# Optimization experiments

Measured on AMD Instinct MI355X. Metric: run time of the kernel, lower is better.

The kernel has to match this reference:

```python
import jax, jax.numpy as jnp
import numpy as np

COMMITMENT_COST = 0.25
FMAX = jnp.finfo(jnp.float32).max


def _vq(x, codebook, commitment_cost):
    """Eval-mode VectorQuantizerEMA forward. x: [T, B, D], codebook: [K, D]."""
    K, D = codebook.shape
    flat = x.reshape(-1, D)  # [N, D]
    dist = (jnp.sum(flat * flat, axis=1, keepdims=True)
            + jnp.sum(codebook * codebook, axis=1)
            - 2.0 * flat @ codebook.T)
    idx = jnp.argmin(dist, axis=1)                      # [N]
    quantized = codebook[idx].reshape(x.shape)          # gather instead of one-hot matmul
    e_latent_loss = jnp.mean((jax.lax.stop_gradient(quantized) - x) ** 2)
    loss = commitment_cost * e_latent_loss
    q_st = x + jax.lax.stop_gradient(quantized - x)     # straight-through
    counts = jnp.zeros((K,), dtype=x.dtype).at[idx].add(1.0)
    avg_probs = counts / flat.shape[0]
    perplexity = jnp.exp(-jnp.sum(avg_probs * jnp.log(avg_probs + 1e-10)))
    return loss, q_st, perplexity, idx, dist


def setup_inputs() -> dict:
    key = jax.random.key(0)
    k1, k2, k3 = jax.random.split(key, 3)
    Tp1, B, D = 257, 64, 768
    Kc, Kf = 512, 4096
    return {
        "features": jax.random.normal(k1, (Tp1, B, D), dtype=jnp.float32),
        "class_codebook": jax.random.normal(k2, (Kc, D), dtype=jnp.float32),
        "feat_codebook": jax.random.normal(k3, (Kf, D), dtype=jnp.float32),
    }


def reference(features, class_codebook, feat_codebook):
    Kc = class_codebook.shape[0]
    Kf = feat_codebook.shape[0]
    B = features.shape[1]

    # class quantization on features[0][None] -> [1, B, D]
    c_loss, q_class, c_perp, c_idx, c_dist = _vq(features[0][None], class_codebook, COMMITMENT_COST)
    # feature quantization on features[1:] -> [T, B, D]
    f_loss, q_feat, f_perp, f_idx, f_dist = _vq(features[1:], feat_codebook, COMMITMENT_COST)

    T = q_feat.shape[0]
    class_indices = c_idx.reshape(1, B)
    feature_indices = (f_idx + Kc).reshape(T, B)

    class_distances = c_dist.reshape(1, B, Kc)
    feature_distances = f_dist.reshape(T, B, Kf)
    # pad each with float32 max so argmin stays within own codebook range
    class_distances = jnp.concatenate(
        [class_distances, jnp.full((1, B, Kf), FMAX, dtype=jnp.float32)], axis=-1)
    feature_distances = jnp.concatenate(
        [jnp.full((T, B, Kc), FMAX, dtype=jnp.float32), feature_distances], axis=-1)
    distances = jnp.concatenate([class_distances, feature_distances], axis=0)  # [T+1, B, Kc+Kf]
    distances = jnp.transpose(distances, (1, 0, 2))                            # [B, T+1, Kc+Kf]

    encoding_indices = jnp.concatenate([class_indices, feature_indices], axis=0).reshape(-1, 1)
    quantized_features = jnp.concatenate([q_class, q_feat], axis=0)            # [T+1, B, D]

    loss = f_loss + c_loss
    perplexity = f_perp + c_perp
    return loss, quantized_features, perplexity, encoding_indices, distances
```

## Files before the change

kernel.cpp:

```cpp
#include <hip/hip_runtime.h>
#include <math.h>

#define DD 768
#define BB 64
#define TT 256
#define TP1 257
#define KCLS 512
#define KFEAT 4096
#define KSUM 4608
#define NROW_F 16384
#define NROW_ALL 16448

#define OFF_Q 1
#define OFF_PERP 12632065
#define OFF_IDX 12632066
#define OFF_DIST 12648514
#define PADV 3.0e38f

#define WS_COUNTS 0
#define WS_LOSS 4608
#define WS_XSQ 4736
#define WS_ESQ 21184
#define WSB_AMIN 103168ULL
#define WSB_AH   234752ULL
#define WSB_BH   25400576ULL

typedef __attribute__((ext_vector_type(8))) short bf16x8;
typedef __attribute__((ext_vector_type(4))) float f32x4;
typedef unsigned long long u64;

__device__ __forceinline__ unsigned short f2bf(float f) {
  unsigned u = __float_as_uint(f);
  unsigned r = (u + 0x7fff + ((u >> 16) & 1)) >> 16;
  return (unsigned short)r;
}
__device__ __forceinline__ void gload16(void* l, const void* g) {
  __builtin_amdgcn_global_load_lds((const __attribute__((address_space(1))) void*)g,
                                   (__attribute__((address_space(3))) void*)l, 16, 0, 0);
}

#define NA4 3145728
#define NB4 786432
__global__ __launch_bounds__(256) void convert_k(const float* __restrict__ A,
                                                 const float* __restrict__ B,
                                                 ushort* __restrict__ Ah,
                                                 ushort* __restrict__ Bh) {
  int i = blockIdx.x * 256 + threadIdx.x;
  const float4* src; ushort* dh; int j;
  if (i < NA4) { src = (const float4*)A; j = i; dh = Ah; }
  else { src = (const float4*)B; j = i - NA4; dh = Bh; }
  float4 v = src[j];
  ushort4 h;
  h.x = f2bf(v.x); h.y = f2bf(v.y); h.z = f2bf(v.z); h.w = f2bf(v.w);
  ((ushort4*)dh)[j] = h;
}

__global__ __launch_bounds__(256) void norms_k(const float* __restrict__ feats,
                                               const float* __restrict__ ccb,
                                               const float* __restrict__ fcb,
                                               float* __restrict__ ws) {
  int wv = (blockIdx.x << 2) + (threadIdx.x >> 6);
  int lane = threadIdx.x & 63;
  const float* src; float* dst;
  if (wv < NROW_ALL) { src = feats + (size_t)wv * DD; dst = ws + WS_XSQ + wv; }
  else if (wv < NROW_ALL + KCLS) { int j = wv - NROW_ALL; src = ccb + (size_t)j * DD; dst = ws + WS_ESQ + j; }
  else { int j = wv - (NROW_ALL + KCLS); src = fcb + (size_t)j * DD; dst = ws + WS_ESQ + KCLS + j; }
  const float4* s4 = (const float4*)src;
  float s = 0.f;
#pragma unroll
  for (int i = 0; i < 3; ++i) {
    float4 v = s4[lane + (i << 6)];
    s = fmaf(v.x, v.x, s); s = fmaf(v.y, v.y, s);
    s = fmaf(v.z, v.z, s); s = fmaf(v.w, v.w, s);
  }
  for (int off = 32; off; off >>= 1) s += __shfl_down(s, off, 64);
  if (lane == 0) *dst = s;
}

__global__ __launch_bounds__(256) void fill_fmax(float* __restrict__ out) {
  int i = blockIdx.x * 256 + threadIdx.x;
  if (i < BB * KFEAT) {
    int b = i >> 12, k = i & 4095;
    out[OFF_DIST + (size_t)b * TP1 * KSUM + KCLS + k] = PADV;
  } else {
    int j = i - BB * KFEAT;
    int b = j / (TT * KCLS);
    int rem = j % (TT * KCLS);
    int t = rem >> 9, k = rem & 511;
    out[OFF_DIST + ((size_t)b * TP1 + 1 + t) * KSUM + k] = PADV;
  }
}

#define GT 128
#define GK 32
__global__ __launch_bounds__(256) void gemm_mfma(const ushort* __restrict__ Ah,
                                                 const ushort* __restrict__ Bh,
                                                 const float* __restrict__ xsq,
                                                 const float* __restrict__ esq,
                                                 u64* __restrict__ amin,
                                                 float* __restrict__ out) {
  __shared__ ushort sA[GT * GK], sB[GT * GK];
  const int t = threadIdx.x;
  const int m0 = blockIdx.x * GT, n0 = blockIdx.y * GT;
  const int L = t & 63, w = t >> 6;
  const int wm = w & 1, wn = w >> 1;
  const int lr = L & 15, q = L >> 4;

  f32x4 acc[4][4];
#pragma unroll
  for (int i = 0; i < 4; ++i)
#pragma unroll
    for (int j = 0; j < 4; ++j) acc[i][j] = (f32x4){0.f, 0.f, 0.f, 0.f};

  const int row0 = t >> 2, kc = t & 3;
  const ushort* gA0 = Ah + (size_t)(m0 + row0) * DD + kc * 8;
  const ushort* gB0 = Bh + (size_t)(n0 + row0) * DD + kc * 8;
  const int wb0 = (w * 64) * 16;
  const int wb1 = (256 + w * 64) * 16;

  const int aoff = (wm * 64 + lr) * GK + q * 8;
  const int boff = (wn * 64 + lr) * GK + q * 8;

  for (int k0 = 0; k0 < DD; k0 += GK) {
    __syncthreads();
    gload16((char*)sA + wb0, gA0 + k0);
    gload16((char*)sA + wb1, gA0 + (size_t)64 * DD + k0);
    gload16((char*)sB + wb0, gB0 + k0);
    gload16((char*)sB + wb1, gB0 + (size_t)64 * DD + k0);
    __syncthreads();

    bf16x8 va[4], vb[4];
#pragma unroll
    for (int f = 0; f < 4; ++f) {
      va[f] = *(const bf16x8*)(sA + aoff + f * 16 * GK);
      vb[f] = *(const bf16x8*)(sB + boff + f * 16 * GK);
    }
#pragma unroll
    for (int fi = 0; fi < 4; ++fi)
#pragma unroll
      for (int fj = 0; fj < 4; ++fj)
        acc[fi][fj] = __builtin_amdgcn_mfma_f32_16x16x32_bf16(va[fi], vb[fj], acc[fi][fj], 0, 0, 0);
  }

  float es[4];
#pragma unroll
  for (int fj = 0; fj < 4; ++fj) es[fj] = esq[n0 + wn * 64 + fj * 16 + lr];

#pragma unroll
  for (int fi = 0; fi < 4; ++fi) {
#pragma unroll
    for (int reg = 0; reg < 4; ++reg) {
      int m = m0 + wm * 64 + fi * 16 + q * 4 + reg;
      float xs = xsq[m];
      int tt = m >> 6, b = m & 63;
      float* orow = out + OFF_DIST + ((size_t)b * TP1 + 1 + tt) * KSUM + KCLS + n0 + wn * 64;
      u64 best = 0xFFFFFFFFFFFFFFFFULL;
#pragma unroll
      for (int fj = 0; fj < 4; ++fj) {
        int nl = fj * 16 + lr;
        float d = xs + es[fj] - 2.f * acc[fi][fj][reg];
        orow[nl] = d;
        u64 pk = ((u64)__float_as_uint(d) << 32) | (unsigned)(n0 + wn * 64 + nl);
        best = pk < best ? pk : best;
      }
#pragma unroll
      for (int msk = 1; msk < 16; msk <<= 1) {
        u64 o = __shfl_xor(best, msk, 64);
        best = o < best ? o : best;
      }
      if (lr == 0) atomicMin(&amin[m], best);
    }
  }
}

__global__ __launch_bounds__(256) void class_dist(const float* __restrict__ X,
                                                  const float* __restrict__ C,
                                                  const float* __restrict__ xsq,
                                                  const float* __restrict__ esq,
                                                  u64* __restrict__ amin,
                                                  float* __restrict__ out) {
  int wv = (blockIdx.x << 2) + (threadIdx.x >> 6);
  int lane = threadIdx.x & 63;
  int row = wv >> 9, col = wv & 511;
  const float4* x4 = (const float4*)(X + (size_t)row * DD);
  const float4* c4 = (const float4*)(C + (size_t)col * DD);
  float s = 0.f;
#pragma unroll
  for (int i = 0; i < 3; ++i) {
    float4 a = x4[lane + (i << 6)];
    float4 b = c4[lane + (i << 6)];
    s = fmaf(a.x, b.x, s); s = fmaf(a.y, b.y, s);
    s = fmaf(a.z, b.z, s); s = fmaf(a.w, b.w, s);
  }
  for (int off = 32; off; off >>= 1) s += __shfl_down(s, off, 64);
  if (lane == 0) {
    float d = xsq[row] + esq[col] - 2.f * s;
    out[OFF_DIST + (size_t)row * TP1 * KSUM + col] = d;
    u64 pk = ((u64)__float_as_uint(d) << 32) | (unsigned)col;
    atomicMin(&amin[row], pk);
  }
}

#define DELTA 3.0f
__global__ __launch_bounds__(256) void refine_k(const float* __restrict__ feats,
                                                const float* __restrict__ fcb,
                                                const float* __restrict__ xsqF,
                                                const float* __restrict__ esqF,
                                                u64* __restrict__ aminF,
                                                const float* __restrict__ out) {
  const int r = blockIdx.x;
  const int tid = threadIdx.x;
  const int tt = r >> 6, b = r & 63;
  const float* drow = out + OFF_DIST + ((size_t)b * TP1 + 1 + tt) * KSUM + KCLS;
  u64 p0 = aminF[r];
  float dmin = __uint_as_float((unsigned)(p0 >> 32));
  float thr = dmin + DELTA;

  __shared__ int cnt;
  __shared__ int cand[64];
  __shared__ float red[256];
  if (tid == 0) cnt = 0;
  __syncthreads();

  const float2* d2 = (const float2*)drow;
#pragma unroll
  for (int i = 0; i < 8; ++i) {
    int idx = tid + (i << 8);
    float2 v = d2[idx];
    if (v.x <= thr) { int s = atomicAdd(&cnt, 1); if (s < 64) cand[s] = idx * 2; }
    if (v.y <= thr) { int s = atomicAdd(&cnt, 1); if (s < 64) cand[s] = idx * 2 + 1; }
  }
  __syncthreads();
  int n = cnt < 64 ? cnt : 64;

  const float* xr = feats + (size_t)(BB + r) * DD;
  const float xs = xsqF[r];
  u64 best = 0xFFFFFFFFFFFFFFFFULL;
  for (int ci = 0; ci < n; ++ci) {
    int col = cand[ci];
    const float* er = fcb + (size_t)col * DD;
    float s = 0.f;
#pragma unroll
    for (int k = 0; k < 3; ++k) {
      int e = tid + (k << 8);
      s = fmaf(xr[e], er[e], s);
    }
    red[tid] = s;
    __syncthreads();
    for (int st = 128; st; st >>= 1) { if (tid < st) red[tid] += red[tid + st]; __syncthreads(); }
    float d = xs + esqF[col] - 2.f * red[0];
    u64 pk = ((u64)__float_as_uint(d) << 32) | (unsigned)col;
    best = pk < best ? pk : best;
    __syncthreads();
  }
  if (tid == 0) aminF[r] = best;
}

__global__ __launch_bounds__(256) void finalize2(const float* __restrict__ feats,
                                                 const float* __restrict__ ccb,
                                                 const float* __restrict__ fcb,
                                                 float* __restrict__ out,
                                                 float* __restrict__ ws,
                                                 const u64* __restrict__ amin) {
  int r = blockIdx.x, tid = threadIdx.x;
  u64 p = amin[r];
  int col = (int)(p & 0xFFFFFFFFULL);
  const float* cb; int cbase;
  if (r < BB) { cb = ccb; cbase = 0; } else { cb = fcb; cbase = KCLS; }
  const float4* e4 = (const float4*)(cb + (size_t)col * DD);
  const float4* x4 = (const float4*)(feats + (size_t)r * DD);
  float* qrow = out + OFF_Q + (size_t)r * DD;
  float ls = 0.f;
  if (tid < 192) {
    float4 e = e4[tid]; float4 x = x4[tid];
    qrow[tid * 4 + 0] = e.x; qrow[tid * 4 + 1] = e.y;
    qrow[tid * 4 + 2] = e.z; qrow[tid * 4 + 3] = e.w;
    float dx = e.x - x.x, dy = e.y - x.y, dz = e.z - x.z, dw = e.w - x.w;
    ls = dx * dx + dy * dy + dz * dz + dw * dw;
  }
  __shared__ float sm[256];
  sm[tid] = ls;
  __syncthreads();
  for (int s = 128; s; s >>= 1) { if (tid < s) sm[tid] += sm[tid + s]; __syncthreads(); }
  if (tid == 0) {
    int slot = (r < BB) ? (r & 63) : (64 + (r & 63));
    atomicAdd(&ws[WS_LOSS + slot], sm[0]);
    atomicAdd(&ws[WS_COUNTS + cbase + col], 1.0f);
    out[OFF_IDX + r] = (float)(cbase + col);
  }
}

__global__ __launch_bounds__(256) void perp_k(float* __restrict__ out, const float* __restrict__ ws) {
  int tid = threadIdx.x;
  float ec = 0.f, ef = 0.f;
  for (int k = tid; k < KCLS; k += 256) {
    float p = ws[WS_COUNTS + k] * (1.0f / BB);
    ec += p * logf(p + 1e-10f);
  }
  for (int k = tid; k < KFEAT; k += 256) {
    float p = ws[WS_COUNTS + KCLS + k] * (1.0f / NROW_F);
    ef += p * logf(p + 1e-10f);
  }
  __shared__ float sc[256], sf[256], sl[128];
  sc[tid] = ec; sf[tid] = ef;
  if (tid < 128) sl[tid] = ws[WS_LOSS + tid];
  __syncthreads();
  for (int s = 128; s; s >>= 1) {
    if (tid < s) { sc[tid] += sc[tid + s]; sf[tid] += sf[tid + s]; }
    __syncthreads();
  }
  for (int s = 32; s; s >>= 1) {
    if (tid < s) { sl[tid] += sl[tid + s]; sl[64 + tid] += sl[64 + tid + s]; }
    __syncthreads();
  }
  if (tid == 0) {
    out[OFF_PERP] = expf(-sc[0]) + expf(-sf[0]);
    out[0] = 0.25f * (sl[0] / (float)(BB * DD)) +
             0.25f * (sl[64] / (float)(NROW_F * DD));
  }
}

extern "C" void kernel_launch(void* const* d_in, const int* in_sizes, int n_in,
                              void* d_out, int out_size, void* d_ws, size_t ws_size,
                              hipStream_t stream) {
  const float* feats = (const float*)d_in[0];
  const float* ccb = (const float*)d_in[1];
  const float* fcb = (const float*)d_in[2];
  float* out = (float*)d_out;
  float* ws = (float*)d_ws;
  u64* amin = (u64*)((char*)d_ws + WSB_AMIN);
  ushort* Ah = (ushort*)((char*)d_ws + WSB_AH);
  ushort* Bh = (ushort*)((char*)d_ws + WSB_BH);

  hipMemsetAsync(d_ws, 0, (WS_LOSS + 128) * sizeof(float), stream);
  hipMemsetAsync((char*)d_ws + WSB_AMIN, 0xFF, NROW_ALL * sizeof(u64), stream);
  hipLaunchKernelGGL(convert_k, dim3(15360), dim3(256), 0, stream,
                     feats + (size_t)BB * DD, fcb, Ah, Bh);
  hipLaunchKernelGGL(norms_k, dim3(5264), dim3(256), 0, stream, feats, ccb, fcb, ws);
  hipLaunchKernelGGL(fill_fmax, dim3(33792), dim3(256), 0, stream, out);
  hipLaunchKernelGGL(gemm_mfma, dim3(128, 32), dim3(256), 0, stream,
                     Ah, Bh, ws + WS_XSQ + BB, ws + WS_ESQ + KCLS, amin + BB, out);
  hipLaunchKernelGGL(class_dist, dim3(8192), dim3(256), 0, stream, feats, ccb,
                     ws + WS_XSQ, ws + WS_ESQ, amin, out);
  hipLaunchKernelGGL(refine_k, dim3(16384), dim3(256), 0, stream,
                     feats, fcb, ws + WS_XSQ + BB, ws + WS_ESQ + KCLS, amin + BB, out);
  hipLaunchKernelGGL(finalize2, dim3(16448), dim3(256), 0, stream, feats, ccb, fcb, out, ws, amin);
  hipLaunchKernelGGL(perp_k, dim3(1), dim3(256), 0, stream, out, ws);
}
```

Baseline: 920.1 us.

## Fuse prep and finalize kernels, double-buffer and swizzle GEMM LDS, nontemporal stores

Merges the bf16 conversion into the norms kernel, so the inputs are read once. Fuses the refine and finalize steps for feature rows, with per-wave candidate dot products replacing the block-wide reductions. The GEMM gets double-buffered LDS staging with an XOR swizzle to overlap loads with MFMA and reduce bank conflicts. The large distance and padding writes use nontemporal stores to limit cache pollution. The swizzle has to agree between the global-load and LDS-read indexing, and the stages must stay correctly synchronized.

```diff
diff --git a/kernel.cpp b/kernel.cpp
--- a/kernel.cpp
+++ b/kernel.cpp
@@ -39,39 +39,37 @@
                                    (__attribute__((address_space(3))) void*)l, 16, 0, 0);
 }
 
-#define NA4 3145728
-#define NB4 786432
-__global__ __launch_bounds__(256) void convert_k(const float* __restrict__ A,
-                                                 const float* __restrict__ B,
-                                                 ushort* __restrict__ Ah,
-                                                 ushort* __restrict__ Bh) {
-  int i = blockIdx.x * 256 + threadIdx.x;
-  const float4* src; ushort* dh; int j;
-  if (i < NA4) { src = (const float4*)A; j = i; dh = Ah; }
-  else { src = (const float4*)B; j = i - NA4; dh = Bh; }
-  float4 v = src[j];
-  ushort4 h;
-  h.x = f2bf(v.x); h.y = f2bf(v.y); h.z = f2bf(v.z); h.w = f2bf(v.w);
-  ((ushort4*)dh)[j] = h;
-}
-
-__global__ __launch_bounds__(256) void norms_k(const float* __restrict__ feats,
-                                               const float* __restrict__ ccb,
-                                               const float* __restrict__ fcb,
-                                               float* __restrict__ ws) {
+__global__ __launch_bounds__(256) void prep_k(const float* __restrict__ feats,
+                                              const float* __restrict__ ccb,
+                                              const float* __restrict__ fcb,
+                                              float* __restrict__ ws,
+                                              ushort* __restrict__ Ah,
+                                              ushort* __restrict__ Bh) {
   int wv = (blockIdx.x << 2) + (threadIdx.x >> 6);
   int lane = threadIdx.x & 63;
-  const float* src; float* dst;
-  if (wv < NROW_ALL) { src = feats + (size_t)wv * DD; dst = ws + WS_XSQ + wv; }
-  else if (wv < NROW_ALL + KCLS) { int j = wv - NROW_ALL; src = ccb + (size_t)j * DD; dst = ws + WS_ESQ + j; }
-  else { int j = wv - (NROW_ALL + KCLS); src = fcb + (size_t)j * DD; dst = ws + WS_ESQ + KCLS + j; }
+  const float* src; float* dst; ushort* bh = nullptr;
+  if (wv < NROW_ALL) {
+    src = feats + (size_t)wv * DD; dst = ws + WS_XSQ + wv;
+    if (wv >= BB) bh = Ah + (size_t)(wv - BB) * DD;
+  } else if (wv < NROW_ALL + KCLS) {
+    int j = wv - NROW_ALL; src = ccb + (size_t)j * DD; dst = ws + WS_ESQ + j;
+  } else {
+    int j = wv - (NROW_ALL + KCLS); src = fcb + (size_t)j * DD; dst = ws + WS_ESQ + KCLS + j;
+    bh = Bh + (size_t)j * DD;
+  }
   const float4* s4 = (const float4*)src;
+  ushort4* b4 = (ushort4*)bh;
   float s = 0.f;
 #pragma unroll
   for (int i = 0; i < 3; ++i) {
     float4 v = s4[lane + (i << 6)];
     s = fmaf(v.x, v.x, s); s = fmaf(v.y, v.y, s);
     s = fmaf(v.z, v.z, s); s = fmaf(v.w, v.w, s);
+    if (bh) {
+      ushort4 h;
+      h.x = f2bf(v.x); h.y = f2bf(v.y); h.z = f2bf(v.z); h.w = f2bf(v.w);
+      b4[lane + (i << 6)] = h;
+    }
   }
   for (int off = 32; off; off >>= 1) s += __shfl_down(s, off, 64);
   if (lane == 0) *dst = s;
@@ -81,25 +79,47 @@
   int i = blockIdx.x * 256 + threadIdx.x;
   if (i < BB * KFEAT) {
     int b = i >> 12, k = i & 4095;
-    out[OFF_DIST + (size_t)b * TP1 * KSUM + KCLS + k] = PADV;
+    __builtin_nontemporal_store(PADV, &out[OFF_DIST + (size_t)b * TP1 * KSUM + KCLS + k]);
   } else {
     int j = i - BB * KFEAT;
     int b = j / (TT * KCLS);
     int rem = j % (TT * KCLS);
     int t = rem >> 9, k = rem & 511;
-    out[OFF_DIST + ((size_t)b * TP1 + 1 + t) * KSUM + k] = PADV;
+    __builtin_nontemporal_store(PADV, &out[OFF_DIST + ((size_t)b * TP1 + 1 + t) * KSUM + k]);
   }
 }
 
 #define GT 128
 #define GK 32
+
+#define STAGE(bA, bB, koff) do { \
+    gload16((char*)(bA) + wb0, gA0 + (koff)); \
+    gload16((char*)(bA) + wb1, gA0 + (size_t)64 * DD + (koff)); \
+    gload16((char*)(bB) + wb0, gB0 + (koff)); \
+    gload16((char*)(bB) + wb1, gB0 + (size_t)64 * DD + (koff)); \
+  } while (0)
+
+#define COMPUTE(bA, bB) do { \
+    bf16x8 va[4], vb[4]; \
+    _Pragma("unroll") \
+    for (int f = 0; f < 4; ++f) { \
+      va[f] = *(const bf16x8*)((bA) + aoff + f * 16 * GK); \
+      vb[f] = *(const bf16x8*)((bB) + boff + f * 16 * GK); \
+    } \
+    _Pragma("unroll") \
+    for (int fi = 0; fi < 4; ++fi) \
+      _Pragma("unroll") \
+      for (int fj = 0; fj < 4; ++fj) \
+        acc[fi][fj] = __builtin_amdgcn_mfma_f32_16x16x32_bf16(va[fi], vb[fj], acc[fi][fj], 0, 0, 0); \
+  } while (0)
+
 __global__ __launch_bounds__(256) void gemm_mfma(const ushort* __restrict__ Ah,
                                                  const ushort* __restrict__ Bh,
                                                  const float* __restrict__ xsq,
                                                  const float* __restrict__ esq,
                                                  u64* __restrict__ amin,
                                                  float* __restrict__ out) {
-  __shared__ ushort sA[GT * GK], sB[GT * GK];
+  __shared__ ushort sA[2][GT * GK], sB[2][GT * GK];
   const int t = threadIdx.x;
   const int m0 = blockIdx.x * GT, n0 = blockIdx.y * GT;
   const int L = t & 63, w = t >> 6;
@@ -112,34 +132,27 @@
 #pragma unroll
     for (int j = 0; j < 4; ++j) acc[i][j] = (f32x4){0.f, 0.f, 0.f, 0.f};
 
-  const int row0 = t >> 2, kc = t & 3;
-  const ushort* gA0 = Ah + (size_t)(m0 + row0) * DD + kc * 8;
-  const ushort* gB0 = Bh + (size_t)(n0 + row0) * DD + kc * 8;
+  const int row0 = t >> 2;
+  const int kcs = (t & 3) ^ ((t >> 3) & 3);
+  const ushort* gA0 = Ah + (size_t)(m0 + row0) * DD + kcs * 8;
+  const ushort* gB0 = Bh + (size_t)(n0 + row0) * DD + kcs * 8;
   const int wb0 = (w * 64) * 16;
   const int wb1 = (256 + w * 64) * 16;
 
-  const int aoff = (wm * 64 + lr) * GK + q * 8;
-  const int boff = (wn * 64 + lr) * GK + q * 8;
-
-  for (int k0 = 0; k0 < DD; k0 += GK) {
+  const int qs = q ^ ((lr >> 1) & 3);
+  const int aoff = (wm * 64 + lr) * GK + qs * 8;
+  const int boff = (wn * 64 + lr) * GK + qs * 8;
+
+  STAGE(sA[0], sB[0], 0);
+  __syncthreads();
+
+  for (int k0 = 0; k0 < DD; k0 += 2 * GK) {
+    if (k0 + GK < DD) STAGE(sA[1], sB[1], k0 + GK);
+    COMPUTE(sA[0], sB[0]);
     __syncthreads();
-    gload16((char*)sA + wb0, gA0 + k0);
-    gload16((char*)sA + wb1, gA0 + (size_t)64 * DD + k0);
-    gload16((char*)sB + wb0, gB0 + k0);
-    gload16((char*)sB + wb1, gB0 + (size_t)64 * DD + k0);
+    if (k0 + 2 * GK < DD) STAGE(sA[0], sB[0], k0 + 2 * GK);
+    COMPUTE(sA[1], sB[1]);
     __syncthreads();
-
-    bf16x8 va[4], vb[4];
-#pragma unroll
-    for (int f = 0; f < 4; ++f) {
-      va[f] = *(const bf16x8*)(sA + aoff + f * 16 * GK);
-      vb[f] = *(const bf16x8*)(sB + boff + f * 16 * GK);
-    }
-#pragma unroll
-    for (int fi = 0; fi < 4; ++fi)
-#pragma unroll
-      for (int fj = 0; fj < 4; ++fj)
-        acc[fi][fj] = __builtin_amdgcn_mfma_f32_16x16x32_bf16(va[fi], vb[fj], acc[fi][fj], 0, 0, 0);
   }
 
   float es[4];
@@ -159,7 +172,7 @@
       for (int fj = 0; fj < 4; ++fj) {
         int nl = fj * 16 + lr;
         float d = xs + es[fj] - 2.f * acc[fi][fj][reg];
-        orow[nl] = d;
+        __builtin_nontemporal_store(d, &orow[nl]);
         u64 pk = ((u64)__float_as_uint(d) << 32) | (unsigned)(n0 + wn * 64 + nl);
         best = pk < best ? pk : best;
       }
@@ -202,23 +215,26 @@
 }
 
 #define DELTA 3.0f
-__global__ __launch_bounds__(256) void refine_k(const float* __restrict__ feats,
-                                                const float* __restrict__ fcb,
-                                                const float* __restrict__ xsqF,
-                                                const float* __restrict__ esqF,
-                                                u64* __restrict__ aminF,
-                                                const float* __restrict__ out) {
+__global__ __launch_bounds__(256) void refine_fin(const float* __restrict__ feats,
+                                                  const float* __restrict__ fcb,
+                                                  const float* __restrict__ xsqF,
+                                                  const float* __restrict__ esqF,
+                                                  const u64* __restrict__ aminF,
+                                                  float* __restrict__ out,
+                                                  float* __restrict__ ws) {
   const int r = blockIdx.x;
   const int tid = threadIdx.x;
+  const int lane = tid & 63, wv = tid >> 6;
   const int tt = r >> 6, b = r & 63;
   const float* drow = out + OFF_DIST + ((size_t)b * TP1 + 1 + tt) * KSUM + KCLS;
   u64 p0 = aminF[r];
-  float dmin = __uint_as_float((unsigned)(p0 >> 32));
-  float thr = dmin + DELTA;
+  float thr = __uint_as_float((unsigned)(p0 >> 32)) + DELTA;
 
   __shared__ int cnt;
   __shared__ int cand[64];
-  __shared__ float red[256];
+  __shared__ u64 wbest[4];
+  __shared__ float wls[4];
+  __shared__ int wincol;
   if (tid == 0) cnt = 0;
   __syncthreads();
 
@@ -234,40 +250,69 @@
   int n = cnt < 64 ? cnt : 64;
 
   const float* xr = feats + (size_t)(BB + r) * DD;
+  const float4* x4 = (const float4*)xr;
   const float xs = xsqF[r];
+
   u64 best = 0xFFFFFFFFFFFFFFFFULL;
-  for (int ci = 0; ci < n; ++ci) {
+  for (int ci = wv; ci < n; ci += 4) {
     int col = cand[ci];
-    const float* er = fcb + (size_t)col * DD;
+    const float4* e4 = (const float4*)(fcb + (size_t)col * DD);
     float s = 0.f;
 #pragma unroll
-    for (int k = 0; k < 3; ++k) {
-      int e = tid + (k << 8);
-      s = fmaf(xr[e], er[e], s);
+    for (int i = 0; i < 3; ++i) {
+      float4 a = x4[lane + (i << 6)];
+      float4 e = e4[lane + (i << 6)];
+      s = fmaf(a.x, e.x, s); s = fmaf(a.y, e.y, s);
+      s = fmaf(a.z, e.z, s); s = fmaf(a.w, e.w, s);
     }
-    red[tid] = s;
-    __syncthreads();
-    for (int st = 128; st; st >>= 1) { if (tid < st) red[tid] += red[tid + st]; __syncthreads(); }
-    float d = xs + esqF[col] - 2.f * red[0];
-    u64 pk = ((u64)__float_as_uint(d) << 32) | (unsigned)col;
-    best = pk < best ? pk : best;
-    __syncthreads();
-  }
-  if (tid == 0) aminF[r] = best;
-}
-
-__global__ __launch_bounds__(256) void finalize2(const float* __restrict__ feats,
-                                                 const float* __restrict__ ccb,
-                                                 const float* __restrict__ fcb,
-                                                 float* __restrict__ out,
-                                                 float* __restrict__ ws,
-                                                 const u64* __restrict__ amin) {
+    for (int off = 32; off; off >>= 1) s += __shfl_down(s, off, 64);
+    if (lane == 0) {
+      float d = xs + esqF[col] - 2.f * s;
+      u64 pk = ((u64)__float_as_uint(d) << 32) | (unsigned)col;
+      best = pk < best ? pk : best;
+    }
+  }
+  if (lane == 0) wbest[wv] = best;
+  __syncthreads();
+  if (tid == 0) {
+    u64 bb = wbest[0];
+    if (wbest[1] < bb) bb = wbest[1];
+    if (wbest[2] < bb) bb = wbest[2];
+    if (wbest[3] < bb) bb = wbest[3];
+    wincol = (int)(bb & 0xFFFFFFFFULL);
+  }
+  __syncthreads();
+  const int col = wincol;
+
+  const float4* e4 = (const float4*)(fcb + (size_t)col * DD);
+  float* qrow = out + OFF_Q + (size_t)(BB + r) * DD;
+  float ls = 0.f;
+  if (tid < 192) {
+    float4 e = e4[tid]; float4 x = x4[tid];
+    qrow[tid * 4 + 0] = e.x; qrow[tid * 4 + 1] = e.y;
+    qrow[tid * 4 + 2] = e.z; qrow[tid * 4 + 3] = e.w;
+    float dx = e.x - x.x, dy = e.y - x.y, dz = e.z - x.z, dw = e.w - x.w;
+    ls = dx * dx + dy * dy + dz * dz + dw * dw;
+  }
+  for (int off = 32; off; off >>= 1) ls += __shfl_down(ls, off, 64);
+  if (lane == 0) wls[wv] = ls;
+  __syncthreads();
+  if (tid == 0) {
+    atomicAdd(&ws[WS_LOSS + 64 + (r & 63)], wls[0] + wls[1] + wls[2] + wls[3]);
+    atomicAdd(&ws[WS_COUNTS + KCLS + col], 1.0f);
+    out[OFF_IDX + BB + r] = (float)(KCLS + col);
+  }
+}
+
+__global__ __launch_bounds__(256) void final_class(const float* __restrict__ feats,
+                                                   const float* __restrict__ ccb,
+                                                   float* __restrict__ out,
+                                                   float* __restrict__ ws,
+                                                   const u64* __restrict__ amin) {
   int r = blockIdx.x, tid = threadIdx.x;
-  u64 p = amin[r];
-  int col = (int)(p & 0xFFFFFFFFULL);
-  const float* cb; int cbase;
-  if (r < BB) { cb = ccb; cbase = 0; } else { cb = fcb; cbase = KCLS; }
-  const float4* e4 = (const float4*)(cb + (size_t)col * DD);
+  int lane = tid & 63, wv = tid >> 6;
+  int col = (int)(amin[r] & 0xFFFFFFFFULL);
+  const float4* e4 = (const float4*)(ccb + (size_t)col * DD);
   const float4* x4 = (const float4*)(feats + (size_t)r * DD);
   float* qrow = out + OFF_Q + (size_t)r * DD;
   float ls = 0.f;
@@ -278,15 +323,14 @@
     float dx = e.x - x.x, dy = e.y - x.y, dz = e.z - x.z, dw = e.w - x.w;
     ls = dx * dx + dy * dy + dz * dz + dw * dw;
   }
-  __shared__ float sm[256];
-  sm[tid] = ls;
-  __syncthreads();
-  for (int s = 128; s; s >>= 1) { if (tid < s) sm[tid] += sm[tid + s]; __syncthreads(); }
+  __shared__ float wls[4];
+  for (int off = 32; off; off >>= 1) ls += __shfl_down(ls, off, 64);
+  if (lane == 0) wls[wv] = ls;
+  __syncthreads();
   if (tid == 0) {
-    int slot = (r < BB) ? (r & 63) : (64 + (r & 63));
-    atomicAdd(&ws[WS_LOSS + slot], sm[0]);
-    atomicAdd(&ws[WS_COUNTS + cbase + col], 1.0f);
-    out[OFF_IDX + r] = (float)(cbase + col);
+    atomicAdd(&ws[WS_LOSS + (r & 63)], wls[0] + wls[1] + wls[2] + wls[3]);
+    atomicAdd(&ws[WS_COUNTS + col], 1.0f);
+    out[OFF_IDX + r] = (float)col;
   }
 }
 
@@ -334,16 +378,14 @@
 
   hipMemsetAsync(d_ws, 0, (WS_LOSS + 128) * sizeof(float), stream);
   hipMemsetAsync((char*)d_ws + WSB_AMIN, 0xFF, NROW_ALL * sizeof(u64), stream);
-  hipLaunchKernelGGL(convert_k, dim3(15360), dim3(256), 0, stream,
-                     feats + (size_t)BB * DD, fcb, Ah, Bh);
-  hipLaunchKernelGGL(norms_k, dim3(5264), dim3(256), 0, stream, feats, ccb, fcb, ws);
+  hipLaunchKernelGGL(prep_k, dim3(5264), dim3(256), 0, stream, feats, ccb, fcb, ws, Ah, Bh);
   hipLaunchKernelGGL(fill_fmax, dim3(33792), dim3(256), 0, stream, out);
   hipLaunchKernelGGL(gemm_mfma, dim3(128, 32), dim3(256), 0, stream,
                      Ah, Bh, ws + WS_XSQ + BB, ws + WS_ESQ + KCLS, amin + BB, out);
   hipLaunchKernelGGL(class_dist, dim3(8192), dim3(256), 0, stream, feats, ccb,
                      ws + WS_XSQ, ws + WS_ESQ, amin, out);
-  hipLaunchKernelGGL(refine_k, dim3(16384), dim3(256), 0, stream,
-                     feats, fcb, ws + WS_XSQ + BB, ws + WS_ESQ + KCLS, amin + BB, out);
-  hipLaunchKernelGGL(finalize2, dim3(16448), dim3(256), 0, stream, feats, ccb, fcb, out, ws, amin);
+  hipLaunchKernelGGL(refine_fin, dim3(16384), dim3(256), 0, stream,
+                     feats, fcb, ws + WS_XSQ + BB, ws + WS_ESQ + KCLS, amin + BB, out, ws);
+  hipLaunchKernelGGL(final_class, dim3(64), dim3(256), 0, stream, feats, ccb, out, ws, amin);
   hipLaunchKernelGGL(perp_k, dim3(1), dim3(256), 0, stream, out, ws);
 }
```

New measurement: 858.9 us. -6.7%, faster.
